# Kernel optimization log

Hardware: AMD Instinct MI355X
Metric: run time of the kernel (lower is better)

Reference implementation:

```python
import jax, jax.numpy as jnp
import numpy as np

B, S, D, H = 2, 2048, 1024, 16
DH = D // H
LEVELS, FACTOR = 3, 2


def setup_inputs() -> dict:
    key = jax.random.key(0)
    ks = jax.random.split(key, 12)
    s = 1.0 / np.sqrt(D)
    n = lambda k, shape, sc: (jax.random.normal(k, shape, jnp.float32) * sc)
    return {
        "query": n(ks[0], (B, S, D), 1.0),
        "key": n(ks[1], (B, S, D), 1.0),
        "value": n(ks[2], (B, S, D), 1.0),
        "Wq": n(ks[3], (D, D), s), "bq": jnp.zeros((D,), jnp.float32),
        "Wk": n(ks[4], (D, D), s), "bk": jnp.zeros((D,), jnp.float32),
        "Wv": n(ks[5], (D, D), s), "bv": jnp.zeros((D,), jnp.float32),
        "Wo": n(ks[6], (D, D), s), "bo": jnp.zeros((D,), jnp.float32),
        "w_levels": jnp.ones((LEVELS,), jnp.float32),
    }


def _downsample(m):
    # mean-pool pairs along sequence: [B, S, D] -> [B, S//FACTOR, D]
    b, s, d = m.shape
    sn = s // FACTOR
    return m[:, : sn * FACTOR, :].reshape(b, sn, FACTOR, d).mean(axis=2)


def _mha(q, k, v, Wq, bq, Wk, bk, Wv, bv, Wo, bo):
    b, sq, d = q.shape
    sk = k.shape[1]
    qh = (q @ Wq + bq).reshape(b, sq, H, DH)
    kh = (k @ Wk + bk).reshape(b, sk, H, DH)
    vh = (v @ Wv + bv).reshape(b, sk, H, DH)
    scores = jnp.einsum("bqhd,bkhd->bhqk", qh, kh) / np.sqrt(DH)
    attn = jax.nn.softmax(scores, axis=-1)
    out = jnp.einsum("bhqk,bkhd->bqhd", attn, vh).reshape(b, sq, d)
    return out @ Wo + bo


def reference(query, key, value, Wq, bq, Wk, bk, Wv, bv, Wo, bo, w_levels):
    keys, vals = [key], [value]
    k_, v_ = key, value
    for _ in range(LEVELS - 1):
        k_ = _downsample(k_)
        v_ = _downsample(v_)
        keys.append(k_)
        vals.append(v_)
    acc = None
    for lvl in range(LEVELS):
        o = _mha(query, keys[lvl], vals[lvl], Wq, bq, Wk, bk, Wv, bv, Wo, bo)
        o = o * w_levels[lvl]
        acc = o if acc is None else acc + o
    return acc / w_levels.sum()
```

## Files before the change

kernel.cpp:

```cpp
#include <hip/hip_runtime.h>


#define B_  2
#define S_  2048
#define D_  1024
#define H_  16
#define DH_ 64
#define THR2 10.0f

typedef short s8v __attribute__((ext_vector_type(8)));
typedef float f4v __attribute__((ext_vector_type(4)));
typedef float f16v __attribute__((ext_vector_type(16)));
typedef unsigned int u32x2 __attribute__((ext_vector_type(2)));
typedef unsigned int u32x4 __attribute__((ext_vector_type(4)));

__device__ __forceinline__ unsigned cvtpk(float lo, float hi){
    unsigned r;
    asm volatile("v_cvt_pk_bf16_f32 %0, %1, %2" : "=v"(r) : "v"(lo), "v"(hi));
    return r;
}
__device__ __forceinline__ unsigned short f2bf1(float v){
    unsigned r;
    asm volatile("v_cvt_pk_bf16_f32 %0, %1, %2" : "=v"(r) : "v"(v), "v"(v));
    return (unsigned short)r;
}
__device__ __forceinline__ float bf2f(unsigned short h){
    union { unsigned u; float f; } v; v.u = ((unsigned)h) << 16;
    return v.f;
}
__device__ __forceinline__ float exp2_(float x){
    float r; asm("v_exp_f32 %0, %1" : "=v"(r) : "v"(x)); return r;
}
__device__ __forceinline__ float max3_(float a, float b, float c){
    float r; asm("v_max3_f32 %0, %1, %2, %3" : "=v"(r) : "v"(a), "v"(b), "v"(c));
    return r;
}
__device__ __forceinline__ void pswap(unsigned &dst, unsigned &src){
    asm volatile("v_permlane32_swap_b32 %0, %1" : "+v"(dst), "+v"(src));
}
__device__ __forceinline__ unsigned addpk3(unsigned x, unsigned y, unsigned z){
    union { unsigned u; float f; } xl, yl, zl, xh, yh, zh;
    xl.u = x << 16;          yl.u = y << 16;          zl.u = z << 16;
    xh.u = x & 0xFFFF0000u;  yh.u = y & 0xFFFF0000u;  zh.u = z & 0xFFFF0000u;
    return cvtpk(xl.f + yl.f + zl.f, xh.f + yh.f + zh.f);
}
__device__ __forceinline__ int swz(int row, int kb){
    return row*128 + (((kb) ^ (row & 7) ^ ((row >> 3) & 7)) << 4);
}

__global__ __launch_bounds__(256) void wtrans(
    const float* __restrict__ W0, const float* __restrict__ W1,
    const float* __restrict__ W2, const float* __restrict__ W3,
    unsigned short* __restrict__ T0, unsigned short* __restrict__ T1,
    unsigned short* __restrict__ T2, unsigned short* __restrict__ T3)
{
    __shared__ float tl[32][33];
    const float* W = blockIdx.z==0?W0: blockIdx.z==1?W1: blockIdx.z==2?W2:W3;
    unsigned short* T = blockIdx.z==0?T0: blockIdx.z==1?T1: blockIdx.z==2?T2:T3;
    const int t = threadIdx.x;
    const int bk = blockIdx.x*32, bn = blockIdx.y*32;
    {
        int row = t>>3, c4 = (t&7)*4;
        float4 v = *(const float4*)&W[(size_t)(bk+row)*D_ + bn + c4];
        tl[row][c4+0]=v.x; tl[row][c4+1]=v.y; tl[row][c4+2]=v.z; tl[row][c4+3]=v.w;
    }
    __syncthreads();
    {
        int n = t>>3, k4 = (t&7)*4;
        unsigned a = cvtpk(tl[k4+0][n], tl[k4+1][n]);
        unsigned b = cvtpk(tl[k4+2][n], tl[k4+3][n]);
        u32x2 pk = {a, b};
        *(u32x2*)&T[(size_t)(bn+n)*D_ + bk + k4] = pk;
    }
}

__global__ __launch_bounds__(256) void gemm_qkv3(
    const float* __restrict__ Aq, const float* __restrict__ Ak, const float* __restrict__ Avv,
    const unsigned short* __restrict__ Wq_, const unsigned short* __restrict__ Wk_,
    const unsigned short* __restrict__ Wv_,
    const float* __restrict__ bq_, const float* __restrict__ bk_, const float* __restrict__ bv_,
    unsigned short* __restrict__ Oq, unsigned short* __restrict__ Ok,
    unsigned short* __restrict__ Ov, float scale_q)
{
    const int z = blockIdx.z;
    const float* Af = z==0?Aq : z==1?Ak : Avv;
    const unsigned short* Btw = z==0?Wq_ : z==1?Wk_ : Wv_;
    const float* bias = z==0?bq_ : z==1?bk_ : bv_;
    unsigned short* C = z==0?Oq : z==1?Ok : Ov;
    const float scale = z==0? scale_q : 1.0f;

    const int N_ = D_, K_ = D_;
    __shared__ __align__(16) char lds[65536];
    const int t = threadIdx.x;
    const int l = t & 63, wvi = t>>6, g = l>>4, x = l&15;
    const int wr = wvi>>1, wc = wvi&1;
    const int br = blockIdx.y*128, bc = blockIdx.x*128;

    int rw[4], bl[4];
    #pragma unroll
    for (int p=0;p<4;++p){ int u = t + 256*p; rw[p] = u>>3; bl[p] = u&7; }

    f4v acc[4][4];
    #pragma unroll
    for (int i=0;i<4;++i)
        #pragma unroll
        for (int j=0;j<4;++j) acc[i][j] = (f4v){0.f,0.f,0.f,0.f};

    float4 alo[4], ahi[4]; s8v brg[4];
    #pragma unroll
    for (int p=0;p<4;++p){
        const float* ap = Af + (size_t)(br+rw[p])*K_ + bl[p]*8;
        alo[p] = *(const float4*)ap; ahi[p] = *(const float4*)(ap+4);
        brg[p] = *(const s8v*)(Btw + (size_t)(bc+rw[p])*K_ + bl[p]*8);
    }

    int cur = 0;
    for (int kt=0; kt<K_; kt+=64){
        char* AsB = lds + cur*32768;
        char* BsB = AsB + 16384;
        #pragma unroll
        for (int p=0;p<4;++p){
            uint4 pk;
            pk.x = cvtpk(alo[p].x, alo[p].y); pk.y = cvtpk(alo[p].z, alo[p].w);
            pk.z = cvtpk(ahi[p].x, ahi[p].y); pk.w = cvtpk(ahi[p].z, ahi[p].w);
            *(uint4*)(AsB + swz(rw[p], bl[p])) = pk;
            *(s8v*)(BsB + swz(rw[p], bl[p])) = brg[p];
        }
        if (kt + 64 < K_){
            #pragma unroll
            for (int p=0;p<4;++p){
                const float* ap = Af + (size_t)(br+rw[p])*K_ + (kt+64) + bl[p]*8;
                alo[p] = *(const float4*)ap; ahi[p] = *(const float4*)(ap+4);
                brg[p] = *(const s8v*)(Btw + (size_t)(bc+rw[p])*K_ + (kt+64) + bl[p]*8);
            }
        }
        __syncthreads();
        #pragma unroll
        for (int c=0;c<2;++c){
            s8v af[4], bf[4];
            #pragma unroll
            for (int fm=0; fm<4; ++fm)
                af[fm] = *(const s8v*)(AsB + swz(wr*64+fm*16+x, c*4+g));
            #pragma unroll
            for (int fn=0; fn<4; ++fn)
                bf[fn] = *(const s8v*)(BsB + swz(wc*64+fn*16+x, c*4+g));
            __builtin_amdgcn_s_setprio(1);
            #pragma unroll
            for (int fm=0; fm<4; ++fm)
                #pragma unroll
                for (int fn=0; fn<4; ++fn)
                    acc[fm][fn] = __builtin_amdgcn_mfma_f32_16x16x32_bf16(
                        af[fm], bf[fn], acc[fm][fn], 0,0,0);
            __builtin_amdgcn_s_setprio(0);
        }
        cur ^= 1;
    }

    #pragma unroll
    for (int fn=0; fn<4; ++fn){
        int col = bc + wc*64 + fn*16 + x;
        float bv = bias[col];
        #pragma unroll
        for (int fm=0; fm<4; ++fm){
            int row0 = br + wr*64 + fm*16 + g*4;
            float v0 = acc[fm][fn][0] + bv;
            float v1 = acc[fm][fn][1] + bv;
            float v2 = acc[fm][fn][2] + bv;
            float v3 = acc[fm][fn][3] + bv;
            if (z != 2){
                int hI = col>>6, dhI = col & (DH_-1);
                #pragma unroll
                for (int r=0;r<4;++r){
                    int row = row0 + r;
                    int bI = row>>11, sI = row & (S_-1);
                    float vv = (r==0?v0: r==1?v1: r==2?v2: v3) * scale;
                    C[(((size_t)(bI*H_+hI))*S_+sI)*DH_+dhI] = f2bf1(vv);
                }
            } else {
                int bI = row0>>11, sI = row0 & (S_-1);
                int hI = col>>6, dhI = col & (DH_-1);
                u32x2 pk;
                pk.x = cvtpk(v0, v1);
                pk.y = cvtpk(v2, v3);
                *(u32x2*)&C[(((size_t)(bI*H_+hI))*DH_+dhI)*S_ + sI] = pk;
            }
        }
    }
}

__global__ __launch_bounds__(256) void gemm_sum(
    const unsigned short* __restrict__ A0, const unsigned short* __restrict__ A1,
    const unsigned short* __restrict__ A2, const unsigned short* __restrict__ Btw,
    const float* __restrict__ bias, float* __restrict__ C)
{
    const int N_ = D_, K_ = D_;
    __shared__ __align__(16) char lds[65536];
    const int t = threadIdx.x;
    const int l = t & 63, wvi = t>>6, g = l>>4, x = l&15;
    const int wr = wvi>>1, wc = wvi&1;
    const int br = blockIdx.y*128, bc = blockIdx.x*128;

    int rw[4], bl[4];
    #pragma unroll
    for (int p=0;p<4;++p){ int u = t + 256*p; rw[p] = u>>3; bl[p] = u&7; }

    f4v acc[4][4];
    #pragma unroll
    for (int i=0;i<4;++i)
        #pragma unroll
        for (int j=0;j<4;++j) acc[i][j] = (f4v){0.f,0.f,0.f,0.f};

    u32x4 a0r[4], a1r[4], a2r[4]; s8v brg[4];
    #pragma unroll
    for (int p=0;p<4;++p){
        size_t off = (size_t)(br+rw[p])*K_ + bl[p]*8;
        a0r[p] = *(const u32x4*)(A0 + off);
        a1r[p] = *(const u32x4*)(A1 + off);
        a2r[p] = *(const u32x4*)(A2 + off);
        brg[p] = *(const s8v*)(Btw + (size_t)(bc+rw[p])*K_ + bl[p]*8);
    }

    int cur = 0;
    for (int kt=0; kt<K_; kt+=64){
        char* AsB = lds + cur*32768;
        char* BsB = AsB + 16384;
        #pragma unroll
        for (int p=0;p<4;++p){
            uint4 pk;
            pk.x = addpk3(a0r[p].x, a1r[p].x, a2r[p].x);
            pk.y = addpk3(a0r[p].y, a1r[p].y, a2r[p].y);
            pk.z = addpk3(a0r[p].z, a1r[p].z, a2r[p].z);
            pk.w = addpk3(a0r[p].w, a1r[p].w, a2r[p].w);
            *(uint4*)(AsB + swz(rw[p], bl[p])) = pk;
            *(s8v*)(BsB + swz(rw[p], bl[p])) = brg[p];
        }
        if (kt + 64 < K_){
            #pragma unroll
            for (int p=0;p<4;++p){
                size_t off = (size_t)(br+rw[p])*K_ + (kt+64) + bl[p]*8;
                a0r[p] = *(const u32x4*)(A0 + off);
                a1r[p] = *(const u32x4*)(A1 + off);
                a2r[p] = *(const u32x4*)(A2 + off);
                brg[p] = *(const s8v*)(Btw + (size_t)(bc+rw[p])*K_ + (kt+64) + bl[p]*8);
            }
        }
        __syncthreads();
        #pragma unroll
        for (int c=0;c<2;++c){
            s8v af[4], bf[4];
            #pragma unroll
            for (int fm=0; fm<4; ++fm)
                af[fm] = *(const s8v*)(AsB + swz(wr*64+fm*16+x, c*4+g));
            #pragma unroll
            for (int fn=0; fn<4; ++fn)
                bf[fn] = *(const s8v*)(BsB + swz(wc*64+fn*16+x, c*4+g));
            __builtin_amdgcn_s_setprio(1);
            #pragma unroll
            for (int fm=0; fm<4; ++fm)
                #pragma unroll
                for (int fn=0; fn<4; ++fn)
                    acc[fm][fn] = __builtin_amdgcn_mfma_f32_16x16x32_bf16(
                        af[fm], bf[fn], acc[fm][fn], 0,0,0);
            __builtin_amdgcn_s_setprio(0);
        }
        cur ^= 1;
    }

    #pragma unroll
    for (int fn=0; fn<4; ++fn){
        int col = bc + wc*64 + fn*16 + x;
        float bv = bias[col];
        #pragma unroll
        for (int fm=0; fm<4; ++fm){
            int row0 = br + wr*64 + fm*16 + g*4;
            #pragma unroll
            for (int r=0;r<4;++r)
                C[(size_t)(row0+r)*N_ + col] = acc[fm][fn][r] + bv;
        }
    }
}

__global__ __launch_bounds__(256) void pool_pair(
    const unsigned short* __restrict__ kin, unsigned short* __restrict__ kout,
    const unsigned short* __restrict__ vin, unsigned short* __restrict__ vout,
    int nOut4, int Sin, int shift)
{
    int idx = blockIdx.x * 256 + threadIdx.x;
    if (idx >= nOut4) return;
    if (blockIdx.z == 0){
        int d0 = (idx & 15) * 4;
        int rest = idx >> 4;
        int Sout = Sin >> 1;
        int so = rest % Sout, bh = rest / Sout;
        size_t base = ((size_t)bh * Sin + 2*so) * DH_ + d0;
        ushort4 a = *(const ushort4*)&kin[base];
        ushort4 c = *(const ushort4*)&kin[base + DH_];
        ushort4 o;
        o.x = f2bf1(0.5f*(bf2f(a.x)+bf2f(c.x)));
        o.y = f2bf1(0.5f*(bf2f(a.y)+bf2f(c.y)));
        o.z = f2bf1(0.5f*(bf2f(a.z)+bf2f(c.z)));
        o.w = f2bf1(0.5f*(bf2f(a.w)+bf2f(c.w)));
        *(ushort4*)&kout[(size_t)idx*4] = o;
    } else {
        int row = idx >> shift;
        int so4 = (idx & ((1<<shift)-1)) << 2;
        union { u32x4 u; unsigned short hh[8]; } a;
        a.u = *(const u32x4*)&vin[(size_t)row*Sin + so4*2];
        float m0 = 0.5f*(bf2f(a.hh[0])+bf2f(a.hh[1]));
        float m1 = 0.5f*(bf2f(a.hh[2])+bf2f(a.hh[3]));
        float m2 = 0.5f*(bf2f(a.hh[4])+bf2f(a.hh[5]));
        float m3 = 0.5f*(bf2f(a.hh[6])+bf2f(a.hh[7]));
        u32x2 pk; pk.x = cvtpk(m0,m1); pk.y = cvtpk(m2,m3);
        *(u32x2*)&vout[(size_t)row*(Sin>>1) + so4] = pk;
    }
}

__global__ __launch_bounds__(256, 3) void attn_mfma8(
    const unsigned short* __restrict__ qh,
    const unsigned short* __restrict__ kh0, const unsigned short* __restrict__ kh1,
    const unsigned short* __restrict__ kh2,
    const unsigned short* __restrict__ vt0, const unsigned short* __restrict__ vt1,
    const unsigned short* __restrict__ vt2,
    const float* __restrict__ wlv,
    unsigned short* __restrict__ acc0, unsigned short* __restrict__ acc1,
    unsigned short* __restrict__ acc2)
{
    __shared__ __align__(16) char ksm[2][8192];
    __shared__ __align__(16) char vsm[2][8192];
    const int t = threadIdx.x, l = t&63, wv = t>>6, q = l&31, hi = l>>5;
    const int bid = blockIdx.x;
    const int qt = bid & 15, h = (bid>>4) & (H_-1), b = bid >> 8;
    const int lvl = blockIdx.y;
    const int nt = 32 >> lvl;
    const unsigned short* kp  = lvl==0 ? kh0 : (lvl==1 ? kh1 : kh2);
    const unsigned short* vpt = lvl==0 ? vt0 : (lvl==1 ? vt1 : vt2);
    unsigned short* accOut    = lvl==0 ? acc0 : (lvl==1 ? acc1 : acc2);

    const float w0 = wlv[0], w1 = wlv[1], w2 = wlv[2];
    const float wl = wlv[lvl] / (w0 + w1 + w2);

    const unsigned short* qp =
        qh + (((size_t)(b*H_+h))*S_ + (size_t)qt*128 + wv*32 + q)*DH_ + hi*8;
    s8v qf0 = *(const s8v*)(qp);
    s8v qf1 = *(const s8v*)(qp + 16);
    s8v qf2 = *(const s8v*)(qp + 32);
    s8v qf3 = *(const s8v*)(qp + 48);

    const int r0 = t>>3, kb = t&7;
    const int off0 = swz(r0, kb), off1 = swz(r0+32, kb);

    const int Sl = nt*64;
    const unsigned short* kbase = kp + (size_t)(b*H_+h)*Sl*DH_;
    const unsigned short* v0r = vpt + ((size_t)(b*H_+h)*DH_ + r0)*Sl;
    const unsigned short* v1r = vpt + ((size_t)(b*H_+h)*DH_ + r0+32)*Sl;

    float m_i = -1e30f, l_i = 0.f;
    f16v o0, o1;
    #pragma unroll
    for (int r=0;r<16;++r){ o0[r]=0.f; o1[r]=0.f; }

    s8v krg0 = *(const s8v*)(kbase + (size_t)r0*DH_ + kb*8);
    s8v krg1 = *(const s8v*)(kbase + (size_t)(r0+32)*DH_ + kb*8);
    s8v vrg0 = *(const s8v*)(v0r + kb*8);
    s8v vrg1 = *(const s8v*)(v1r + kb*8);

    int cur = 0;
    for (int kt = 0; kt < nt; ++kt) {
        char* kb_ = ksm[cur];
        char* vb_ = vsm[cur];
        *(s8v*)(kb_ + off0) = krg0;
        *(s8v*)(kb_ + off1) = krg1;
        *(s8v*)(vb_ + off0) = vrg0;
        *(s8v*)(vb_ + off1) = vrg1;
        if (kt + 1 < nt) {
            size_t nb = (size_t)(kt+1)*64;
            krg0 = *(const s8v*)(kbase + (nb+r0)*DH_ + kb*8);
            krg1 = *(const s8v*)(kbase + (nb+r0+32)*DH_ + kb*8);
            vrg0 = *(const s8v*)(v0r + nb + kb*8);
            vrg1 = *(const s8v*)(v1r + nb + kb*8);
        }
        __syncthreads();

        f16v s0, s1;
        #pragma unroll
        for (int r=0;r<16;++r){ s0[r]=0.f; s1[r]=0.f; }
        {
            s8v k00 = *(const s8v*)(kb_ + swz(q,      0*2+hi));
            s8v k01 = *(const s8v*)(kb_ + swz(q,      1*2+hi));
            s8v k02 = *(const s8v*)(kb_ + swz(q,      2*2+hi));
            s8v k03 = *(const s8v*)(kb_ + swz(q,      3*2+hi));
            s8v k10 = *(const s8v*)(kb_ + swz(32+q,   0*2+hi));
            s8v k11 = *(const s8v*)(kb_ + swz(32+q,   1*2+hi));
            s8v k12 = *(const s8v*)(kb_ + swz(32+q,   2*2+hi));
            s8v k13 = *(const s8v*)(kb_ + swz(32+q,   3*2+hi));
            __builtin_amdgcn_s_setprio(1);
            s0 = __builtin_amdgcn_mfma_f32_32x32x16_bf16(k00, qf0, s0, 0,0,0);
            s1 = __builtin_amdgcn_mfma_f32_32x32x16_bf16(k10, qf0, s1, 0,0,0);
            s0 = __builtin_amdgcn_mfma_f32_32x32x16_bf16(k01, qf1, s0, 0,0,0);
            s1 = __builtin_amdgcn_mfma_f32_32x32x16_bf16(k11, qf1, s1, 0,0,0);
            s0 = __builtin_amdgcn_mfma_f32_32x32x16_bf16(k02, qf2, s0, 0,0,0);
            s1 = __builtin_amdgcn_mfma_f32_32x32x16_bf16(k12, qf2, s1, 0,0,0);
            s0 = __builtin_amdgcn_mfma_f32_32x32x16_bf16(k03, qf3, s0, 0,0,0);
            s1 = __builtin_amdgcn_mfma_f32_32x32x16_bf16(k13, qf3, s1, 0,0,0);
            __builtin_amdgcn_s_setprio(0);
        }

        float ca = max3_(s0[0], s0[1], s0[2]);
        ca = max3_(ca, s0[3], s0[4]);
        ca = max3_(ca, s0[5], s0[6]);
        ca = fmaxf(ca, s0[7]);
        float cb = max3_(s0[8], s0[9], s0[10]);
        cb = max3_(cb, s0[11], s0[12]);
        cb = max3_(cb, s0[13], s0[14]);
        cb = fmaxf(cb, s0[15]);
        float cc = max3_(s1[0], s1[1], s1[2]);
        cc = max3_(cc, s1[3], s1[4]);
        cc = max3_(cc, s1[5], s1[6]);
        cc = fmaxf(cc, s1[7]);
        float cd = max3_(s1[8], s1[9], s1[10]);
        cd = max3_(cd, s1[11], s1[12]);
        cd = max3_(cd, s1[13], s1[14]);
        cd = fmaxf(cd, s1[15]);
        float pm = fmaxf(max3_(ca, cb, cc), cd);
        pm = fmaxf(pm, __shfl_xor(pm, 32, 64));
        if (__any(pm > m_i + THR2)) {
            float mn = fmaxf(m_i, pm);
            float corr = exp2_(m_i - mn);
            m_i = mn;
            l_i *= corr;
            #pragma unroll
            for (int r=0;r<16;++r){
                float cbc = __shfl(corr, ((r&3)+8*(r>>2)) + 4*hi, 64);
                o0[r] *= cbc; o1[r] *= cbc;
            }
        }
        float rs = 0.f;
        #pragma unroll
        for (int r=0;r<16;++r){ s0[r] = exp2_(s0[r]-m_i); rs += s0[r]; }
        #pragma unroll
        for (int r=0;r<16;++r){ s1[r] = exp2_(s1[r]-m_i); rs += s1[r]; }
        rs += __shfl_xor(rs, 32, 64);
        l_i += rs;

        unsigned a0 = cvtpk(s0[0], s0[1]),  a1 = cvtpk(s0[2], s0[3]);
        unsigned b0 = cvtpk(s0[4], s0[5]),  b1 = cvtpk(s0[6], s0[7]);
        pswap(a0, b0); pswap(a1, b1);
        unsigned c0 = cvtpk(s0[8], s0[9]),  c1 = cvtpk(s0[10], s0[11]);
        unsigned d0 = cvtpk(s0[12], s0[13]),d1 = cvtpk(s0[14], s0[15]);
        pswap(c0, d0); pswap(c1, d1);
        unsigned e0 = cvtpk(s1[0], s1[1]),  e1 = cvtpk(s1[2], s1[3]);
        unsigned f0 = cvtpk(s1[4], s1[5]),  f1 = cvtpk(s1[6], s1[7]);
        pswap(e0, f0); pswap(e1, f1);
        unsigned g0 = cvtpk(s1[8], s1[9]),  g1 = cvtpk(s1[10], s1[11]);
        unsigned h0 = cvtpk(s1[12], s1[13]),h1 = cvtpk(s1[14], s1[15]);
        pswap(g0, h0); pswap(g1, h1);
        union { u32x4 u; s8v s; } pf0, pf1, pf2, pf3;
        pf0.u = (u32x4){a0, a1, b0, b1};
        pf1.u = (u32x4){c0, c1, d0, d1};
        pf2.u = (u32x4){e0, e1, f0, f1};
        pf3.u = (u32x4){g0, g1, h0, h1};

        {
            s8v v00 = *(const s8v*)(vb_ + swz(q,    0*2+hi));
            s8v v01 = *(const s8v*)(vb_ + swz(q,    1*2+hi));
            s8v v02 = *(const s8v*)(vb_ + swz(q,    2*2+hi));
            s8v v03 = *(const s8v*)(vb_ + swz(q,    3*2+hi));
            s8v v10 = *(const s8v*)(vb_ + swz(32+q, 0*2+hi));
            s8v v11 = *(const s8v*)(vb_ + swz(32+q, 1*2+hi));
            s8v v12 = *(const s8v*)(vb_ + swz(32+q, 2*2+hi));
            s8v v13 = *(const s8v*)(vb_ + swz(32+q, 3*2+hi));
            __builtin_amdgcn_s_setprio(1);
            o0 = __builtin_amdgcn_mfma_f32_32x32x16_bf16(pf0.s, v00, o0, 0,0,0);
            o1 = __builtin_amdgcn_mfma_f32_32x32x16_bf16(pf0.s, v10, o1, 0,0,0);
            o0 = __builtin_amdgcn_mfma_f32_32x32x16_bf16(pf1.s, v01, o0, 0,0,0);
            o1 = __builtin_amdgcn_mfma_f32_32x32x16_bf16(pf1.s, v11, o1, 0,0,0);
            o0 = __builtin_amdgcn_mfma_f32_32x32x16_bf16(pf2.s, v02, o0, 0,0,0);
            o1 = __builtin_amdgcn_mfma_f32_32x32x16_bf16(pf2.s, v12, o1, 0,0,0);
            o0 = __builtin_amdgcn_mfma_f32_32x32x16_bf16(pf3.s, v03, o0, 0,0,0);
            o1 = __builtin_amdgcn_mfma_f32_32x32x16_bf16(pf3.s, v13, o1, 0,0,0);
            __builtin_amdgcn_s_setprio(0);
        }
        cur ^= 1;
    }

    #pragma unroll
    for (int r=0;r<16;++r){
        int qrow = ((r&3)+8*(r>>2)) + 4*hi;
        float lb = __shfl(l_i, qrow, 64);
        float sc = wl / lb;
        size_t row = (size_t)b*S_ + (size_t)qt*128 + wv*32 + qrow;
        accOut[row*D_ + h*DH_ + q]      = f2bf1(o0[r] * sc);
        accOut[row*D_ + h*DH_ + 32 + q] = f2bf1(o1[r] * sc);
    }
}

extern "C" void kernel_launch(void* const* d_in, const int* in_sizes, int n_in,
                              void* d_out, int out_size, void* d_ws, size_t ws_size,
                              hipStream_t stream)
{
    const float* query = (const float*)d_in[0];
    const float* key   = (const float*)d_in[1];
    const float* value = (const float*)d_in[2];
    const float* Wq = (const float*)d_in[3];  const float* bq = (const float*)d_in[4];
    const float* Wk = (const float*)d_in[5];  const float* bk = (const float*)d_in[6];
    const float* Wv = (const float*)d_in[7];  const float* bv = (const float*)d_in[8];
    const float* Wo = (const float*)d_in[9];  const float* bo = (const float*)d_in[10];
    const float* wlv = (const float*)d_in[11];

    char* w = (char*)d_ws;
    unsigned short* qhb  = (unsigned short*)(w);
    unsigned short* khb0 = (unsigned short*)(w + 8388608);
    unsigned short* khb1 = (unsigned short*)(w + 16777216);
    unsigned short* khb2 = (unsigned short*)(w + 20971520);
    unsigned short* vtb0 = (unsigned short*)(w + 23068672);
    unsigned short* vtb1 = (unsigned short*)(w + 31457280);
    unsigned short* vtb2 = (unsigned short*)(w + 35651584);
    unsigned short* Wto  = (unsigned short*)(w + 37748736);
    unsigned short* Wtq  = (unsigned short*)(w + 39845888);
    unsigned short* Wtk  = (unsigned short*)(w + 41943040);
    unsigned short* Wtv  = (unsigned short*)(w + 44040192);
    unsigned short* acc0 = (unsigned short*)(w + 39845888);
    unsigned short* acc1 = (unsigned short*)(w + 48234496);
    unsigned short* acc2 = (unsigned short*)(w + 56623104);

    dim3 bb(256);
    wtrans<<<dim3(32,32,4), bb, 0, stream>>>(Wq, Wk, Wv, Wo, Wtq, Wtk, Wtv, Wto);

    const float scale_q = 0.125f * 1.44269504088896f;
    gemm_qkv3<<<dim3(8, 32, 3), bb, 0, stream>>>(query, key, value,
                                                 Wtq, Wtk, Wtv, bq, bk, bv,
                                                 qhb, khb0, vtb0, scale_q);

    int n1 = B_ * H_ * (S_/2) * DH_ / 4;
    int n2 = B_ * H_ * (S_/4) * DH_ / 4;
    pool_pair<<<dim3(n1/256,1,2), bb, 0, stream>>>(khb0, khb1, vtb0, vtb1, n1, S_,   8);
    pool_pair<<<dim3(n2/256,1,2), bb, 0, stream>>>(khb1, khb2, vtb1, vtb2, n2, S_/2, 7);

    attn_mfma8<<<dim3(512, 3), bb, 0, stream>>>(qhb, khb0, khb1, khb2,
                                                vtb0, vtb1, vtb2, wlv,
                                                acc0, acc1, acc2);

    gemm_sum<<<dim3(8, 32), bb, 0, stream>>>(acc0, acc1, acc2, Wto, bo, (float*)d_out);
}
```

Baseline: 196.2 us.

## Fuse K/V pooling into QKV GEMM, async LDS loads in attention, narrower output tiles

The separate pool_pair kernels are removed. The QKV projection epilogue now writes the mean-pooled level-1 and level-2 K and V directly from fp32 accumulators, which saves two launches and a re-read of K and V. The attention kernel replaces its register-staged global-to-LDS copies with global_load_lds direct loads into a double-buffered LDS region. The output GEMM tile is narrowed to 128x64, doubling the grid to 512 blocks for better CU occupancy. Pooling from fp32 slightly changes rounding compared with pooling from bf16, and the epilogue adds scattered 2-byte stores.

```diff
diff --git a/kernel.cpp b/kernel.cpp
--- a/kernel.cpp
+++ b/kernel.cpp
@@ -46,6 +46,11 @@
 }
 __device__ __forceinline__ int swz(int row, int kb){
     return row*128 + (((kb) ^ (row & 7) ^ ((row >> 3) & 7)) << 4);
+}
+__device__ __forceinline__ void gld16(const void* g, void* l){
+    __builtin_amdgcn_global_load_lds(
+        (const __attribute__((address_space(1))) unsigned int*)g,
+        (__attribute__((address_space(3))) unsigned int*)l, 16, 0, 0);
 }
 
 __global__ __launch_bounds__(256) void wtrans(
@@ -80,7 +85,10 @@
     const unsigned short* __restrict__ Wv_,
     const float* __restrict__ bq_, const float* __restrict__ bk_, const float* __restrict__ bv_,
     unsigned short* __restrict__ Oq, unsigned short* __restrict__ Ok,
-    unsigned short* __restrict__ Ov, float scale_q)
+    unsigned short* __restrict__ Ov,
+    unsigned short* __restrict__ K1, unsigned short* __restrict__ K2,
+    unsigned short* __restrict__ V1, unsigned short* __restrict__ V2,
+    float scale_q)
 {
     const int z = blockIdx.z;
     const float* Af = z==0?Aq : z==1?Ak : Avv;
@@ -167,22 +175,29 @@
             float v1 = acc[fm][fn][1] + bv;
             float v2 = acc[fm][fn][2] + bv;
             float v3 = acc[fm][fn][3] + bv;
+            int bI = row0>>11, sI = row0 & (S_-1);
+            int hI = col>>6,  dhI = col & (DH_-1);
+            size_t bh = (size_t)(bI*H_ + hI);
             if (z != 2){
-                int hI = col>>6, dhI = col & (DH_-1);
-                #pragma unroll
-                for (int r=0;r<4;++r){
-                    int row = row0 + r;
-                    int bI = row>>11, sI = row & (S_-1);
-                    float vv = (r==0?v0: r==1?v1: r==2?v2: v3) * scale;
-                    C[(((size_t)(bI*H_+hI))*S_+sI)*DH_+dhI] = f2bf1(vv);
+                unsigned short* p0 = C + (bh*S_ + sI)*DH_ + dhI;
+                p0[0]      = f2bf1(v0*scale);
+                p0[DH_]    = f2bf1(v1*scale);
+                p0[2*DH_]  = f2bf1(v2*scale);
+                p0[3*DH_]  = f2bf1(v3*scale);
+                if (z == 1){
+                    unsigned short* p1 = K1 + (bh*(S_/2) + (sI>>1))*DH_ + dhI;
+                    p1[0]   = f2bf1((v0+v1)*0.5f);
+                    p1[DH_] = f2bf1((v2+v3)*0.5f);
+                    K2[(bh*(S_/4) + (sI>>2))*DH_ + dhI] = f2bf1((v0+v1+v2+v3)*0.25f);
                 }
             } else {
-                int bI = row0>>11, sI = row0 & (S_-1);
-                int hI = col>>6, dhI = col & (DH_-1);
                 u32x2 pk;
                 pk.x = cvtpk(v0, v1);
                 pk.y = cvtpk(v2, v3);
-                *(u32x2*)&C[(((size_t)(bI*H_+hI))*DH_+dhI)*S_ + sI] = pk;
+                *(u32x2*)&C[(bh*DH_+dhI)*S_ + sI] = pk;
+                float m01 = (v0+v1)*0.5f, m23 = (v2+v3)*0.5f;
+                *(unsigned*)&V1[(bh*DH_+dhI)*(S_/2) + (sI>>1)] = cvtpk(m01, m23);
+                V2[(bh*DH_+dhI)*(S_/4) + (sI>>2)] = f2bf1((m01+m23)*0.5f);
             }
         }
     }
@@ -194,35 +209,38 @@
     const float* __restrict__ bias, float* __restrict__ C)
 {
     const int N_ = D_, K_ = D_;
-    __shared__ __align__(16) char lds[65536];
+    __shared__ __align__(16) char lds[49152];
     const int t = threadIdx.x;
     const int l = t & 63, wvi = t>>6, g = l>>4, x = l&15;
     const int wr = wvi>>1, wc = wvi&1;
-    const int br = blockIdx.y*128, bc = blockIdx.x*128;
+    const int br = blockIdx.y*128, bc = blockIdx.x*64;
 
     int rw[4], bl[4];
     #pragma unroll
     for (int p=0;p<4;++p){ int u = t + 256*p; rw[p] = u>>3; bl[p] = u&7; }
-
-    f4v acc[4][4];
-    #pragma unroll
-    for (int i=0;i<4;++i)
-        #pragma unroll
-        for (int j=0;j<4;++j) acc[i][j] = (f4v){0.f,0.f,0.f,0.f};
-
-    u32x4 a0r[4], a1r[4], a2r[4]; s8v brg[4];
+    int bw[2], bb[2];
+    #pragma unroll
+    for (int p=0;p<2;++p){ int u = t + 256*p; bw[p] = u>>3; bb[p] = u&7; }
+
+    f4v acc[4][2];
+    #pragma unroll
+    for (int i=0;i<4;++i){ acc[i][0] = (f4v){0,0,0,0}; acc[i][1] = (f4v){0,0,0,0}; }
+
+    u32x4 a0r[4], a1r[4], a2r[4]; s8v brg[2];
     #pragma unroll
     for (int p=0;p<4;++p){
         size_t off = (size_t)(br+rw[p])*K_ + bl[p]*8;
         a0r[p] = *(const u32x4*)(A0 + off);
         a1r[p] = *(const u32x4*)(A1 + off);
         a2r[p] = *(const u32x4*)(A2 + off);
-        brg[p] = *(const s8v*)(Btw + (size_t)(bc+rw[p])*K_ + bl[p]*8);
-    }
+    }
+    #pragma unroll
+    for (int p=0;p<2;++p)
+        brg[p] = *(const s8v*)(Btw + (size_t)(bc+bw[p])*K_ + bb[p]*8);
 
     int cur = 0;
     for (int kt=0; kt<K_; kt+=64){
-        char* AsB = lds + cur*32768;
+        char* AsB = lds + cur*24576;
         char* BsB = AsB + 16384;
         #pragma unroll
         for (int p=0;p<4;++p){
@@ -232,8 +250,10 @@
             pk.z = addpk3(a0r[p].z, a1r[p].z, a2r[p].z);
             pk.w = addpk3(a0r[p].w, a1r[p].w, a2r[p].w);
             *(uint4*)(AsB + swz(rw[p], bl[p])) = pk;
-            *(s8v*)(BsB + swz(rw[p], bl[p])) = brg[p];
-        }
+        }
+        #pragma unroll
+        for (int p=0;p<2;++p)
+            *(s8v*)(BsB + swz(bw[p], bb[p])) = brg[p];
         if (kt + 64 < K_){
             #pragma unroll
             for (int p=0;p<4;++p){
@@ -241,24 +261,26 @@
                 a0r[p] = *(const u32x4*)(A0 + off);
                 a1r[p] = *(const u32x4*)(A1 + off);
                 a2r[p] = *(const u32x4*)(A2 + off);
-                brg[p] = *(const s8v*)(Btw + (size_t)(bc+rw[p])*K_ + (kt+64) + bl[p]*8);
             }
+            #pragma unroll
+            for (int p=0;p<2;++p)
+                brg[p] = *(const s8v*)(Btw + (size_t)(bc+bw[p])*K_ + (kt+64) + bb[p]*8);
         }
         __syncthreads();
         #pragma unroll
         for (int c=0;c<2;++c){
-            s8v af[4], bf[4];
+            s8v af[4], bf[2];
             #pragma unroll
             for (int fm=0; fm<4; ++fm)
                 af[fm] = *(const s8v*)(AsB + swz(wr*64+fm*16+x, c*4+g));
             #pragma unroll
-            for (int fn=0; fn<4; ++fn)
-                bf[fn] = *(const s8v*)(BsB + swz(wc*64+fn*16+x, c*4+g));
+            for (int fn=0; fn<2; ++fn)
+                bf[fn] = *(const s8v*)(BsB + swz(wc*32+fn*16+x, c*4+g));
             __builtin_amdgcn_s_setprio(1);
             #pragma unroll
             for (int fm=0; fm<4; ++fm)
                 #pragma unroll
-                for (int fn=0; fn<4; ++fn)
+                for (int fn=0; fn<2; ++fn)
                     acc[fm][fn] = __builtin_amdgcn_mfma_f32_16x16x32_bf16(
                         af[fm], bf[fn], acc[fm][fn], 0,0,0);
             __builtin_amdgcn_s_setprio(0);
@@ -267,8 +289,8 @@
     }
 
     #pragma unroll
-    for (int fn=0; fn<4; ++fn){
-        int col = bc + wc*64 + fn*16 + x;
+    for (int fn=0; fn<2; ++fn){
+        int col = bc + wc*32 + fn*16 + x;
         float bv = bias[col];
         #pragma unroll
         for (int fm=0; fm<4; ++fm){
@@ -280,42 +302,7 @@
     }
 }
 
-__global__ __launch_bounds__(256) void pool_pair(
-    const unsigned short* __restrict__ kin, unsigned short* __restrict__ kout,
-    const unsigned short* __restrict__ vin, unsigned short* __restrict__ vout,
-    int nOut4, int Sin, int shift)
-{
-    int idx = blockIdx.x * 256 + threadIdx.x;
-    if (idx >= nOut4) return;
-    if (blockIdx.z == 0){
-        int d0 = (idx & 15) * 4;
-        int rest = idx >> 4;
-        int Sout = Sin >> 1;
-        int so = rest % Sout, bh = rest / Sout;
-        size_t base = ((size_t)bh * Sin + 2*so) * DH_ + d0;
-        ushort4 a = *(const ushort4*)&kin[base];
-        ushort4 c = *(const ushort4*)&kin[base + DH_];
-        ushort4 o;
-        o.x = f2bf1(0.5f*(bf2f(a.x)+bf2f(c.x)));
-        o.y = f2bf1(0.5f*(bf2f(a.y)+bf2f(c.y)));
-        o.z = f2bf1(0.5f*(bf2f(a.z)+bf2f(c.z)));
-        o.w = f2bf1(0.5f*(bf2f(a.w)+bf2f(c.w)));
-        *(ushort4*)&kout[(size_t)idx*4] = o;
-    } else {
-        int row = idx >> shift;
-        int so4 = (idx & ((1<<shift)-1)) << 2;
-        union { u32x4 u; unsigned short hh[8]; } a;
-        a.u = *(const u32x4*)&vin[(size_t)row*Sin + so4*2];
-        float m0 = 0.5f*(bf2f(a.hh[0])+bf2f(a.hh[1]));
-        float m1 = 0.5f*(bf2f(a.hh[2])+bf2f(a.hh[3]));
-        float m2 = 0.5f*(bf2f(a.hh[4])+bf2f(a.hh[5]));
-        float m3 = 0.5f*(bf2f(a.hh[6])+bf2f(a.hh[7]));
-        u32x2 pk; pk.x = cvtpk(m0,m1); pk.y = cvtpk(m2,m3);
-        *(u32x2*)&vout[(size_t)row*(Sin>>1) + so4] = pk;
-    }
-}
-
-__global__ __launch_bounds__(256, 3) void attn_mfma8(
+__global__ __launch_bounds__(256, 3) void attn_mfma9(
     const unsigned short* __restrict__ qh,
     const unsigned short* __restrict__ kh0, const unsigned short* __restrict__ kh1,
     const unsigned short* __restrict__ kh2,
@@ -325,8 +312,7 @@
     unsigned short* __restrict__ acc0, unsigned short* __restrict__ acc1,
     unsigned short* __restrict__ acc2)
 {
-    __shared__ __align__(16) char ksm[2][8192];
-    __shared__ __align__(16) char vsm[2][8192];
+    __shared__ __align__(16) char ldsA[32768];
     const int t = threadIdx.x, l = t&63, wv = t>>6, q = l&31, hi = l>>5;
     const int bid = blockIdx.x;
     const int qt = bid & 15, h = (bid>>4) & (H_-1), b = bid >> 8;
@@ -346,40 +332,46 @@
     s8v qf2 = *(const s8v*)(qp + 32);
     s8v qf3 = *(const s8v*)(qp + 48);
 
-    const int r0 = t>>3, kb = t&7;
-    const int off0 = swz(r0, kb), off1 = swz(r0+32, kb);
-
     const int Sl = nt*64;
-    const unsigned short* kbase = kp + (size_t)(b*H_+h)*Sl*DH_;
-    const unsigned short* v0r = vpt + ((size_t)(b*H_+h)*DH_ + r0)*Sl;
-    const unsigned short* v1r = vpt + ((size_t)(b*H_+h)*DH_ + r0+32)*Sl;
+    const char* gK = (const char*)(kp + (size_t)(b*H_+h)*Sl*DH_);
+    const char* gV = (const char*)(vpt + (size_t)(b*H_+h)*DH_*Sl);
+
+    const int lr = l>>3, lc = l&7;
+    const int kb0 = lc ^ lr ^ wv;
+    const int kb1 = lc ^ lr ^ (wv+4);
+    const int kOffG0 = (((wv*8+lr)*DH_)    + kb0*8)*2;
+    const int kOffG1 = (((32+wv*8+lr)*DH_) + kb1*8)*2;
+    const int vOffG0 = ((wv*8+lr)*Sl    + kb0*8)*2;
+    const int vOffG1 = ((32+wv*8+lr)*Sl + kb1*8)*2;
+    const int ldsOff0 = wv*1024, ldsOff1 = 4096 + wv*1024;
 
     float m_i = -1e30f, l_i = 0.f;
     f16v o0, o1;
     #pragma unroll
     for (int r=0;r<16;++r){ o0[r]=0.f; o1[r]=0.f; }
 
-    s8v krg0 = *(const s8v*)(kbase + (size_t)r0*DH_ + kb*8);
-    s8v krg1 = *(const s8v*)(kbase + (size_t)(r0+32)*DH_ + kb*8);
-    s8v vrg0 = *(const s8v*)(v0r + kb*8);
-    s8v vrg1 = *(const s8v*)(v1r + kb*8);
+    {
+        char* kB = ldsA;           char* vB = ldsA + 8192;
+        gld16(gK + kOffG0, kB + ldsOff0);
+        gld16(gK + kOffG1, kB + ldsOff1);
+        gld16(gV + vOffG0, vB + ldsOff0);
+        gld16(gV + vOffG1, vB + ldsOff1);
+    }
 
     int cur = 0;
     for (int kt = 0; kt < nt; ++kt) {
-        char* kb_ = ksm[cur];
-        char* vb_ = vsm[cur];
-        *(s8v*)(kb_ + off0) = krg0;
-        *(s8v*)(kb_ + off1) = krg1;
-        *(s8v*)(vb_ + off0) = vrg0;
-        *(s8v*)(vb_ + off1) = vrg1;
+        asm volatile("s_waitcnt vmcnt(0)" ::: "memory");
+        __syncthreads();
         if (kt + 1 < nt) {
-            size_t nb = (size_t)(kt+1)*64;
-            krg0 = *(const s8v*)(kbase + (nb+r0)*DH_ + kb*8);
-            krg1 = *(const s8v*)(kbase + (nb+r0+32)*DH_ + kb*8);
-            vrg0 = *(const s8v*)(v0r + nb + kb*8);
-            vrg1 = *(const s8v*)(v1r + nb + kb*8);
-        }
-        __syncthreads();
+            char* kB = ldsA + (cur^1)*16384;
+            char* vB = kB + 8192;
+            gld16(gK + (size_t)(kt+1)*64*DH_*2 + kOffG0, kB + ldsOff0);
+            gld16(gK + (size_t)(kt+1)*64*DH_*2 + kOffG1, kB + ldsOff1);
+            gld16(gV + (size_t)(kt+1)*128      + vOffG0, vB + ldsOff0);
+            gld16(gV + (size_t)(kt+1)*128      + vOffG1, vB + ldsOff1);
+        }
+        char* kb_ = ldsA + cur*16384;
+        char* vb_ = kb_ + 8192;
 
         f16v s0, s1;
         #pragma unroll
@@ -529,16 +521,12 @@
     const float scale_q = 0.125f * 1.44269504088896f;
     gemm_qkv3<<<dim3(8, 32, 3), bb, 0, stream>>>(query, key, value,
                                                  Wtq, Wtk, Wtv, bq, bk, bv,
-                                                 qhb, khb0, vtb0, scale_q);
-
-    int n1 = B_ * H_ * (S_/2) * DH_ / 4;
-    int n2 = B_ * H_ * (S_/4) * DH_ / 4;
-    pool_pair<<<dim3(n1/256,1,2), bb, 0, stream>>>(khb0, khb1, vtb0, vtb1, n1, S_,   8);
-    pool_pair<<<dim3(n2/256,1,2), bb, 0, stream>>>(khb1, khb2, vtb1, vtb2, n2, S_/2, 7);
-
-    attn_mfma8<<<dim3(512, 3), bb, 0, stream>>>(qhb, khb0, khb1, khb2,
+                                                 qhb, khb0, vtb0,
+                                                 khb1, khb2, vtb1, vtb2, scale_q);
+
+    attn_mfma9<<<dim3(512, 3), bb, 0, stream>>>(qhb, khb0, khb1, khb2,
                                                 vtb0, vtb1, vtb2, wlv,
                                                 acc0, acc1, acc2);
 
-    gemm_sum<<<dim3(8, 32), bb, 0, stream>>>(acc0, acc1, acc2, Wto, bo, (float*)d_out);
-}
+    gemm_sum<<<dim3(16, 32), bb, 0, stream>>>(acc0, acc1, acc2, Wto, bo, (float*)d_out);
+}
```

Measured after the change: 194.9 us. About the same (-0.7%).
